# Performance work log

Hardware: AMD Instinct MI355X
Metric: run time of the kernel (lower is better)

Reference implementation:

```python
import jax, jax.numpy as jnp
import numpy as np

B, C, H, W, D = 4, 64, 64, 64, 4
CQ = C // 8  # query/key channels


def setup_inputs() -> dict:
    key = jax.random.key(0)
    ks = jax.random.split(key, 10)
    x2d = jax.random.normal(ks[0], (B, C, H, W, D), dtype=jnp.float32)
    x3d = jax.random.normal(ks[1], (B, C, H, W, D), dtype=jnp.float32)
    # 1x1 Conv3d weights collapsed to (out_ch, in_ch) matrices + biases
    Wq = jax.random.normal(ks[2], (CQ, C), dtype=jnp.float32) * 0.05
    bq = jax.random.normal(ks[3], (CQ,), dtype=jnp.float32) * 0.05
    Wk = jax.random.normal(ks[4], (CQ, C), dtype=jnp.float32) * 0.05
    bk = jax.random.normal(ks[5], (CQ,), dtype=jnp.float32) * 0.05
    Wv = jax.random.normal(ks[6], (C, C), dtype=jnp.float32) * 0.05
    bv = jax.random.normal(ks[7], (C,), dtype=jnp.float32) * 0.05
    gamma = jax.random.normal(ks[8], (1,), dtype=jnp.float32)
    return {"x2d": x2d, "x3d": x3d, "Wq": Wq, "bq": bq, "Wk": Wk,
            "bk": bk, "Wv": Wv, "bv": bv, "gamma": gamma}


def _conv1x1(Wmat, bias, x):
    # x: (B, C, D, H, W); 1x1x1 Conv3d == channel matmul
    y = jnp.einsum('oc,bcdhw->bodhw', Wmat, x)
    return y + bias[None, :, None, None, None]


def reference(x2d, x3d, Wq, bq, Wk, bk, Wv, bv, gamma):
    x = jnp.transpose(x2d, (0, 1, 4, 2, 3))  # (B, C, D, H, W)
    b, c, d, h, w = x.shape
    n = h * w
    q = _conv1x1(Wq, bq, x).reshape(b, -1, n)   # (B, CQ*D, N)
    k = _conv1x1(Wk, bk, x).reshape(b, -1, n)   # (B, CQ*D, N)
    v = _conv1x1(Wv, bv, x).reshape(b, -1, n)   # (B, C*D, N)
    energy = jnp.einsum('bkn,bkm->bnm', q, k)   # (B, N, N), no scaling (faithful)
    attn = jax.nn.softmax(energy, axis=-1)
    # out[b,c,i] = sum_j attn[b,i,j] * v[b,c,j]
    out = jnp.einsum('bcm,bnm->bcn', v, attn)
    out = out.reshape(b, c, d, h, w)
    out = jnp.transpose(out, (0, 1, 3, 4, 2))   # back to (B, C, H, W, D)
    return gamma * out + x3d
```

## Files before the change

kernel.cpp:

```cpp
#include <hip/hip_runtime.h>
#include <hip/hip_bf16.h>

#define CH 64
#define NN 4096
#define SS 16384

typedef __attribute__((ext_vector_type(8))) short bf16x8;
typedef __attribute__((ext_vector_type(4))) float f32x4;

#define QB_OFF 0
#define KB_OFF 524288
#define VT_OFF 1048576

static __device__ __forceinline__ ushort bfbits(float x) {
    __hip_bfloat16 h = __float2bfloat16(x);
    return *(ushort*)&h;
}

static __device__ __forceinline__ float fexp2(float x) {
#if __has_builtin(__builtin_amdgcn_exp2f)
    return __builtin_amdgcn_exp2f(x);
#else
    return exp2f(x);
#endif
}

static __device__ __forceinline__ void gld_lds16(const ushort* g, ushort* l) {
    __builtin_amdgcn_global_load_lds(
        (const __attribute__((address_space(1))) void*)g,
        (__attribute__((address_space(3))) void*)l, 16, 0, 0);
}

__global__ __launch_bounds__(256) void qkv_kernel(
    const float* __restrict__ x,
    const float* __restrict__ Wq, const float* __restrict__ bq,
    const float* __restrict__ Wk, const float* __restrict__ bk,
    const float* __restrict__ Wv, const float* __restrict__ bv,
    ushort* __restrict__ qb, ushort* __restrict__ kb, ushort* __restrict__ vt)
{
    __shared__ __align__(16) ushort Tqk[128 * 40];
    __shared__ __align__(16) ushort Tv[80 * 144];

    const int blk = blockIdx.x;
    const int xcd = blk & 7, jb = blk >> 3;
    const int b = xcd >> 1;
    const int sup = ((xcd & 1) << 4) | (jb & 15);
    const int og = jb >> 4;
    const int tid = threadIdx.x;
    const int nl = tid >> 2, d = tid & 3;

    const int vcnt = (og < 2) ? 12 : 20;
    const int vo0 = (og == 0) ? 0 : (og == 1) ? 12 : (og == 2) ? 24 : 44;

    const float qscale = (og == 0) ? 1.4426950408889634f : 1.0f;

    const float* xb = x + (size_t)b * CH * SS + sup * 512;

    for (int t = 0; t < 2; ++t) {
        const float* xp = xb + t * 256 + tid;
        float xr[CH];
#pragma unroll
        for (int c = 0; c < CH; ++c) xr[c] = xp[(size_t)c * SS];

        const int slot = 32 * (nl >> 4) + 8 * ((nl >> 2) & 3) + 4 * t + (nl & 3);

        if (og < 2) {
            const float* Wqk = (og == 0) ? Wq : Wk;
            const float* bqk = (og == 0) ? bq : bk;
            ushort* trow = &Tqk[(t * 64 + nl) * 40 + d];
#pragma unroll
            for (int o = 0; o < 8; o += 2) {
                float a0 = bqk[o], a1 = bqk[o + 1];
#pragma unroll
                for (int c = 0; c < CH; ++c) {
                    a0 = fmaf(Wqk[o * CH + c],       xr[c], a0);
                    a1 = fmaf(Wqk[(o + 1) * CH + c], xr[c], a1);
                }
                trow[o * 4]       = bfbits(a0 * qscale);
                trow[(o + 1) * 4] = bfbits(a1 * qscale);
            }
        }
        ushort* vcol = &Tv[d * 144 + slot];
        const float* Wvb = Wv + vo0 * CH;
        const float* bvb = bv + vo0;
        if (og < 2) {
#pragma unroll
            for (int j = 0; j < 12; j += 2) {
                float a0 = bvb[j], a1 = bvb[j + 1];
#pragma unroll
                for (int c = 0; c < CH; ++c) {
                    a0 = fmaf(Wvb[j * CH + c],       xr[c], a0);
                    a1 = fmaf(Wvb[(j + 1) * CH + c], xr[c], a1);
                }
                vcol[(j * 4) * 144]       = bfbits(a0);
                vcol[((j + 1) * 4) * 144] = bfbits(a1);
            }
        } else {
#pragma unroll
            for (int j = 0; j < 20; j += 2) {
                float a0 = bvb[j], a1 = bvb[j + 1];
#pragma unroll
                for (int c = 0; c < CH; ++c) {
                    a0 = fmaf(Wvb[j * CH + c],       xr[c], a0);
                    a1 = fmaf(Wvb[(j + 1) * CH + c], xr[c], a1);
                }
                vcol[(j * 4) * 144]       = bfbits(a0);
                vcol[((j + 1) * 4) * 144] = bfbits(a1);
            }
        }
    }
    __syncthreads();

    if (og < 2) {
        ushort* dst = (og == 0 ? qb : kb);
#pragma unroll
        for (int jj = 0; jj < 2; ++jj) {
            int idx = jj * 256 + tid;
            int row = idx >> 2, seg = idx & 3;
            *(uint4*)(dst + ((size_t)(b * NN + sup * 128 + row)) * 32 + seg * 8)
                = *(const uint4*)&Tqk[row * 40 + seg * 8];
        }
    }
    const int nchunks = vcnt * 64;
    ushort* vout = vt + ((size_t)((b * 32 + sup) * 256 + vo0 * 4)) * 144;
#pragma unroll
    for (int j = 0; j < 5; ++j) {
        int idx = j * 256 + tid;
        if (idx < nchunks) {
            int row = idx >> 4, seg = idx & 15;
            *(uint4*)(vout + (size_t)row * 144 + seg * 8)
                = *(const uint4*)&Tv[row * 144 + seg * 8];
        }
    }
}

__global__ __launch_bounds__(256, 2) void flash_kernel(
    const ushort* __restrict__ qb, const ushort* __restrict__ kb,
    const ushort* __restrict__ vt, const float* __restrict__ x3d,
    const float* __restrict__ gptr, float* __restrict__ out)
{
    __shared__ __align__(16) ushort Vls[2][128 * 144];
    __shared__ float lbuf[4 * 4 * 16];

    const int tid = threadIdx.x;
    const int xcd = blockIdx.x & 7, jb = blockIdx.x >> 3;
    const int b   = xcd >> 1;
    const int r0  = (jb & 63) << 6;
    const int cvh = xcd & 1;
    const int w = tid >> 6, lane = tid & 63, q = lane >> 4, l15 = lane & 15;

    bf16x8 Qf[4];
#pragma unroll
    for (int rt = 0; rt < 4; ++rt)
        Qf[rt] = *(const bf16x8*)(qb + (size_t)(b * NN + r0 + 16 * rt + l15) * 32 + 8 * q);

    f32x4 acc[8][4];
#pragma unroll
    for (int i = 0; i < 8; ++i)
#pragma unroll
        for (int j = 0; j < 4; ++j) acc[i][j] = (f32x4){0.f, 0.f, 0.f, 0.f};
    float l_acc[4] = {0.f, 0.f, 0.f, 0.f};

    const ushort* kgl = kb + (size_t)b * NN * 32 + (16 * w + l15) * 32 + 8 * q;

    const ushort* vgl = vt + ((size_t)(b * 32) * 256 + 128 * cvh) * 144;

#pragma unroll
    for (int i = 0; i < 9; ++i)
        gld_lds16(vgl + (size_t)(i * 256 + tid) * 8,
                  (ushort*)Vls[0] + (i * 256 + tid) * 8);

    bf16x8 Kn0 = *(const bf16x8*)(kgl);
    bf16x8 Kn1 = *(const bf16x8*)(kgl + 2048);

    for (int pt = 0; pt < 32; ++pt) {
        __syncthreads();
        if (pt < 31) {
            const ushort* src = vgl + (size_t)(pt + 1) * 36864;
            ushort* dst = (ushort*)Vls[(pt + 1) & 1];
#pragma unroll
            for (int i = 0; i < 9; ++i)
                gld_lds16(src + (size_t)(i * 256 + tid) * 8, dst + (i * 256 + tid) * 8);
        }
        bf16x8 Ka0 = Kn0, Ka1 = Kn1;
        if (pt < 31) {
            Kn0 = *(const bf16x8*)(kgl + (size_t)(2 * pt + 2) * 2048);
            Kn1 = *(const bf16x8*)(kgl + (size_t)(2 * pt + 3) * 2048);
        }

        f32x4 S0[4], S1[4];
#pragma unroll
        for (int rt = 0; rt < 4; ++rt)
            S0[rt] = __builtin_amdgcn_mfma_f32_16x16x32_bf16(
                Ka0, Qf[rt], (f32x4){0.f, 0.f, 0.f, 0.f}, 0, 0, 0);
#pragma unroll
        for (int rt = 0; rt < 4; ++rt)
            S1[rt] = __builtin_amdgcn_mfma_f32_16x16x32_bf16(
                Ka1, Qf[rt], (f32x4){0.f, 0.f, 0.f, 0.f}, 0, 0, 0);

        bf16x8 Pb[4];
#pragma unroll
        for (int rt = 0; rt < 4; ++rt) {
            float e0 = fexp2(S0[rt][0]), e1 = fexp2(S0[rt][1]);
            float e2 = fexp2(S0[rt][2]), e3 = fexp2(S0[rt][3]);
            float f0 = fexp2(S1[rt][0]), f1 = fexp2(S1[rt][1]);
            float f2 = fexp2(S1[rt][2]), f3 = fexp2(S1[rt][3]);
            l_acc[rt] += ((e0 + e1) + (e2 + e3)) + ((f0 + f1) + (f2 + f3));
            bf16x8 p;
            p[0] = (short)bfbits(e0); p[1] = (short)bfbits(e1);
            p[2] = (short)bfbits(e2); p[3] = (short)bfbits(e3);
            p[4] = (short)bfbits(f0); p[5] = (short)bfbits(f1);
            p[6] = (short)bfbits(f2); p[7] = (short)bfbits(f3);
            Pb[rt] = p;
        }

        const ushort* vb = Vls[pt & 1] + 32 * w + 8 * q;
#pragma unroll
        for (int cvt = 0; cvt < 8; ++cvt) {
            bf16x8 Va = *(const bf16x8*)(vb + (16 * cvt + l15) * 144);
#pragma unroll
            for (int rt = 0; rt < 4; ++rt)
                acc[cvt][rt] = __builtin_amdgcn_mfma_f32_16x16x32_bf16(
                    Va, Pb[rt], acc[cvt][rt], 0, 0, 0);
        }
    }

#pragma unroll
    for (int rt = 0; rt < 4; ++rt) {
        float v = l_acc[rt];
        v += __shfl_xor(v, 16);
        v += __shfl_xor(v, 32);
        if (lane < 16) lbuf[(w * 4 + rt) * 16 + lane] = v;
    }
    __syncthreads();
    const float linv = 1.f / (lbuf[(0 + w) * 16 + l15] + lbuf[(4 + w) * 16 + l15] +
                              lbuf[(8 + w) * 16 + l15] + lbuf[(12 + w) * 16 + l15]);
    const float gl = gptr[0] * linv;

    f32x4* Obuf = (f32x4*)&Vls[0][0];
#pragma unroll
    for (int cvt = 0; cvt < 8; ++cvt) {
        __syncthreads();
#pragma unroll
        for (int rt = 0; rt < 4; ++rt)
            Obuf[(w * 64 + lane) * 5 + rt] = acc[cvt][rt];
        __syncthreads();
        f32x4 o = Obuf[lane * 5 + w];
        o += Obuf[(64 + lane) * 5 + w];
        o += Obuf[(128 + lane) * 5 + w];
        o += Obuf[(192 + lane) * 5 + w];
        size_t addr = ((size_t)(b * CH + 32 * cvh + 4 * cvt + q) * NN
                       + (r0 + 16 * w + l15)) * 4;
        float4 xr = *(const float4*)(x3d + addr);
        float4 res;
        res.x = fmaf(gl, o[0], xr.x);
        res.y = fmaf(gl, o[1], xr.y);
        res.z = fmaf(gl, o[2], xr.z);
        res.w = fmaf(gl, o[3], xr.w);
        *(float4*)(out + addr) = res;
    }
}

extern "C" void kernel_launch(void* const* d_in, const int* in_sizes, int n_in,
                              void* d_out, int out_size, void* d_ws, size_t ws_size,
                              hipStream_t stream)
{
    const float* x2d = (const float*)d_in[0];
    const float* x3d = (const float*)d_in[1];
    const float* Wq  = (const float*)d_in[2];
    const float* bq  = (const float*)d_in[3];
    const float* Wk  = (const float*)d_in[4];
    const float* bk  = (const float*)d_in[5];
    const float* Wv  = (const float*)d_in[6];
    const float* bv  = (const float*)d_in[7];
    const float* gma = (const float*)d_in[8];

    ushort* wsb = (ushort*)d_ws;

    qkv_kernel<<<512, 256, 0, stream>>>(x2d, Wq, bq, Wk, bk, Wv, bv,
                                        wsb + QB_OFF, wsb + KB_OFF, wsb + VT_OFF);
    flash_kernel<<<512, 256, 0, stream>>>(wsb + QB_OFF, wsb + KB_OFF, wsb + VT_OFF,
                                          x3d, gma, (float*)d_out);
}
```

Before: 166.0 us.

## Load V fragments directly from global memory instead of LDS double buffering

Removes the LDS double-buffered V staging and its per-iteration block barrier, so each lane reads its V fragment straight from global memory (relying on L2/L1 caching). Obuf gets its own smaller shared array, which cuts LDS use and may let more blocks fit per CU. It also wraps the MFMA sections in s_setprio and replaces the exp2 builtin with inline v_exp_f32 asm. The risk is higher global-load latency and redundant traffic, since the four waves now each fetch V separately, with nothing prefetching it ahead of use.

```diff
diff --git a/kernel.cpp b/kernel.cpp
--- a/kernel.cpp
+++ b/kernel.cpp
@@ -18,17 +18,9 @@
 }
 
 static __device__ __forceinline__ float fexp2(float x) {
-#if __has_builtin(__builtin_amdgcn_exp2f)
-    return __builtin_amdgcn_exp2f(x);
-#else
-    return exp2f(x);
-#endif
-}
-
-static __device__ __forceinline__ void gld_lds16(const ushort* g, ushort* l) {
-    __builtin_amdgcn_global_load_lds(
-        (const __attribute__((address_space(1))) void*)g,
-        (__attribute__((address_space(3))) void*)l, 16, 0, 0);
+    float r;
+    asm("v_exp_f32 %0, %1" : "=v"(r) : "v"(x));
+    return r;
 }
 
 __global__ __launch_bounds__(256) void qkv_kernel(
@@ -139,8 +131,8 @@
     const ushort* __restrict__ vt, const float* __restrict__ x3d,
     const float* __restrict__ gptr, float* __restrict__ out)
 {
-    __shared__ __align__(16) ushort Vls[2][128 * 144];
     __shared__ float lbuf[4 * 4 * 16];
+    __shared__ __align__(16) f32x4 Obuf[1280];
 
     const int tid = threadIdx.x;
     const int xcd = blockIdx.x & 7, jb = blockIdx.x >> 3;
@@ -163,25 +155,13 @@
 
     const ushort* kgl = kb + (size_t)b * NN * 32 + (16 * w + l15) * 32 + 8 * q;
 
-    const ushort* vgl = vt + ((size_t)(b * 32) * 256 + 128 * cvh) * 144;
-
-#pragma unroll
-    for (int i = 0; i < 9; ++i)
-        gld_lds16(vgl + (size_t)(i * 256 + tid) * 8,
-                  (ushort*)Vls[0] + (i * 256 + tid) * 8);
+    const ushort* vbase = vt + ((size_t)(b * 32) * 256 + 128 * cvh + l15) * 144
+                        + 32 * w + 8 * q;
 
     bf16x8 Kn0 = *(const bf16x8*)(kgl);
     bf16x8 Kn1 = *(const bf16x8*)(kgl + 2048);
 
     for (int pt = 0; pt < 32; ++pt) {
-        __syncthreads();
-        if (pt < 31) {
-            const ushort* src = vgl + (size_t)(pt + 1) * 36864;
-            ushort* dst = (ushort*)Vls[(pt + 1) & 1];
-#pragma unroll
-            for (int i = 0; i < 9; ++i)
-                gld_lds16(src + (size_t)(i * 256 + tid) * 8, dst + (i * 256 + tid) * 8);
-        }
         bf16x8 Ka0 = Kn0, Ka1 = Kn1;
         if (pt < 31) {
             Kn0 = *(const bf16x8*)(kgl + (size_t)(2 * pt + 2) * 2048);
@@ -189,6 +169,7 @@
         }
 
         f32x4 S0[4], S1[4];
+        __builtin_amdgcn_s_setprio(1);
 #pragma unroll
         for (int rt = 0; rt < 4; ++rt)
             S0[rt] = __builtin_amdgcn_mfma_f32_16x16x32_bf16(
@@ -197,6 +178,7 @@
         for (int rt = 0; rt < 4; ++rt)
             S1[rt] = __builtin_amdgcn_mfma_f32_16x16x32_bf16(
                 Ka1, Qf[rt], (f32x4){0.f, 0.f, 0.f, 0.f}, 0, 0, 0);
+        __builtin_amdgcn_s_setprio(0);
 
         bf16x8 Pb[4];
 #pragma unroll
@@ -214,15 +196,17 @@
             Pb[rt] = p;
         }
 
-        const ushort* vb = Vls[pt & 1] + 32 * w + 8 * q;
+        const ushort* vp = vbase + (size_t)pt * 36864;
+        __builtin_amdgcn_s_setprio(1);
 #pragma unroll
         for (int cvt = 0; cvt < 8; ++cvt) {
-            bf16x8 Va = *(const bf16x8*)(vb + (16 * cvt + l15) * 144);
+            bf16x8 Va = *(const bf16x8*)(vp + cvt * 2304);
 #pragma unroll
             for (int rt = 0; rt < 4; ++rt)
                 acc[cvt][rt] = __builtin_amdgcn_mfma_f32_16x16x32_bf16(
                     Va, Pb[rt], acc[cvt][rt], 0, 0, 0);
         }
+        __builtin_amdgcn_s_setprio(0);
     }
 
 #pragma unroll
@@ -237,7 +221,6 @@
                               lbuf[(8 + w) * 16 + l15] + lbuf[(12 + w) * 16 + l15]);
     const float gl = gptr[0] * linv;
 
-    f32x4* Obuf = (f32x4*)&Vls[0][0];
 #pragma unroll
     for (int cvt = 0; cvt < 8; ++cvt) {
         __syncthreads();
```

Result: slower. 182.6 us (+10.0%).

## Software-pipeline QK MFMAs one tile ahead of softmax exp and PV

Applied to the files above, without the earlier changes.

Restructures the attention loop so the QK^T MFMAs for the next key tile are issued after the current tile's exp and bf16 packing, which lets matrix-core work overlap with the transcendental VALU work. K register prefetch now runs two tiles ahead. It also adds s_setprio around MFMA blocks and replaces the exp2 builtin with inline v_exp_f32 asm. In exchange it needs more live registers, which may lower occupancy, and the inline asm hides the exp instruction from the compiler's scheduler.

```diff
diff --git a/kernel.cpp b/kernel.cpp
--- a/kernel.cpp
+++ b/kernel.cpp
@@ -18,11 +18,9 @@
 }
 
 static __device__ __forceinline__ float fexp2(float x) {
-#if __has_builtin(__builtin_amdgcn_exp2f)
-    return __builtin_amdgcn_exp2f(x);
-#else
-    return exp2f(x);
-#endif
+    float r;
+    asm("v_exp_f32 %0, %1" : "=v"(r) : "v"(x));
+    return r;
 }
 
 static __device__ __forceinline__ void gld_lds16(const ushort* g, ushort* l) {
@@ -170,8 +168,23 @@
         gld_lds16(vgl + (size_t)(i * 256 + tid) * 8,
                   (ushort*)Vls[0] + (i * 256 + tid) * 8);
 
-    bf16x8 Kn0 = *(const bf16x8*)(kgl);
-    bf16x8 Kn1 = *(const bf16x8*)(kgl + 2048);
+    bf16x8 Kc0 = *(const bf16x8*)(kgl);
+    bf16x8 Kc1 = *(const bf16x8*)(kgl + 2048);
+    bf16x8 Ka0 = *(const bf16x8*)(kgl + 2 * 2048);
+    bf16x8 Ka1 = *(const bf16x8*)(kgl + 3 * 2048);
+    bf16x8 Kn0, Kn1;
+
+    f32x4 S0[4], S1[4];
+    __builtin_amdgcn_s_setprio(1);
+#pragma unroll
+    for (int rt = 0; rt < 4; ++rt)
+        S0[rt] = __builtin_amdgcn_mfma_f32_16x16x32_bf16(
+            Kc0, Qf[rt], (f32x4){0.f, 0.f, 0.f, 0.f}, 0, 0, 0);
+#pragma unroll
+    for (int rt = 0; rt < 4; ++rt)
+        S1[rt] = __builtin_amdgcn_mfma_f32_16x16x32_bf16(
+            Kc1, Qf[rt], (f32x4){0.f, 0.f, 0.f, 0.f}, 0, 0, 0);
+    __builtin_amdgcn_s_setprio(0);
 
     for (int pt = 0; pt < 32; ++pt) {
         __syncthreads();
@@ -182,21 +195,10 @@
             for (int i = 0; i < 9; ++i)
                 gld_lds16(src + (size_t)(i * 256 + tid) * 8, dst + (i * 256 + tid) * 8);
         }
-        bf16x8 Ka0 = Kn0, Ka1 = Kn1;
-        if (pt < 31) {
-            Kn0 = *(const bf16x8*)(kgl + (size_t)(2 * pt + 2) * 2048);
-            Kn1 = *(const bf16x8*)(kgl + (size_t)(2 * pt + 3) * 2048);
-        }
-
-        f32x4 S0[4], S1[4];
-#pragma unroll
-        for (int rt = 0; rt < 4; ++rt)
-            S0[rt] = __builtin_amdgcn_mfma_f32_16x16x32_bf16(
-                Ka0, Qf[rt], (f32x4){0.f, 0.f, 0.f, 0.f}, 0, 0, 0);
-#pragma unroll
-        for (int rt = 0; rt < 4; ++rt)
-            S1[rt] = __builtin_amdgcn_mfma_f32_16x16x32_bf16(
-                Ka1, Qf[rt], (f32x4){0.f, 0.f, 0.f, 0.f}, 0, 0, 0);
+        if (pt < 30) {
+            Kn0 = *(const bf16x8*)(kgl + (size_t)(2 * pt + 4) * 2048);
+            Kn1 = *(const bf16x8*)(kgl + (size_t)(2 * pt + 5) * 2048);
+        }
 
         bf16x8 Pb[4];
 #pragma unroll
@@ -214,7 +216,22 @@
             Pb[rt] = p;
         }
 
+        if (pt < 31) {
+            __builtin_amdgcn_s_setprio(1);
+#pragma unroll
+            for (int rt = 0; rt < 4; ++rt)
+                S0[rt] = __builtin_amdgcn_mfma_f32_16x16x32_bf16(
+                    Ka0, Qf[rt], (f32x4){0.f, 0.f, 0.f, 0.f}, 0, 0, 0);
+#pragma unroll
+            for (int rt = 0; rt < 4; ++rt)
+                S1[rt] = __builtin_amdgcn_mfma_f32_16x16x32_bf16(
+                    Ka1, Qf[rt], (f32x4){0.f, 0.f, 0.f, 0.f}, 0, 0, 0);
+            __builtin_amdgcn_s_setprio(0);
+            Ka0 = Kn0; Ka1 = Kn1;
+        }
+
         const ushort* vb = Vls[pt & 1] + 32 * w + 8 * q;
+        __builtin_amdgcn_s_setprio(1);
 #pragma unroll
         for (int cvt = 0; cvt < 8; ++cvt) {
             bf16x8 Va = *(const bf16x8*)(vb + (16 * cvt + l15) * 144);
@@ -223,6 +240,7 @@
                 acc[cvt][rt] = __builtin_amdgcn_mfma_f32_16x16x32_bf16(
                     Va, Pb[rt], acc[cvt][rt], 0, 0, 0);
         }
+        __builtin_amdgcn_s_setprio(0);
     }
 
 #pragma unroll
```

Result: no change. 165.5 us (-0.3%).
